# Kernel optimization log

Hardware: AMD Instinct MI355X
Metric: run time of the kernel (lower is better)

The kernel has to match this reference:

```python
import jax, jax.numpy as jnp
import numpy as np

N_X = 32640   # total xlmr subword tokens (64 seqs x 510 tokens)
N_S = 16320   # total stanza word tokens (2 subwords per word)
E = 65280     # dependency edges (bidirectional, avg degree ~4)
D = 768
GCN_DIM = 256
GCN_NUM = 2
POS_DIM = 4
N_UPOS = 17
N_LABEL = 5


def setup_inputs() -> dict:
    key = jax.random.key(0)
    ks = jax.random.split(key, 8)
    x = jax.random.normal(ks[0], (N_X, D), dtype=jnp.float32)
    # mapStanza2Xlmr as segment ids: xlmr token j belongs to stanza word j//2
    seg = jnp.arange(N_X, dtype=jnp.int32) // 2
    edge_index = jax.random.randint(ks[1], (2, E), 0, N_S, dtype=jnp.int32)
    upos_ids = jax.random.randint(ks[2], (N_S,), 0, N_UPOS, dtype=jnp.int32)
    Wc = jax.random.normal(ks[3], (D, GCN_DIM), dtype=jnp.float32) * 0.02
    bc = jnp.zeros((GCN_DIM,), dtype=jnp.float32)
    gcn_W = jax.random.normal(ks[4], (GCN_NUM, GCN_DIM, GCN_DIM), dtype=jnp.float32) * 0.05
    gcn_b = jnp.zeros((GCN_NUM, GCN_DIM), dtype=jnp.float32)
    upos_table = jax.random.normal(ks[5], (N_UPOS, POS_DIM), dtype=jnp.float32)
    Wcls = jax.random.normal(ks[6], (D + GCN_DIM + POS_DIM, N_LABEL), dtype=jnp.float32) * 0.02
    bcls = jnp.zeros((N_LABEL,), dtype=jnp.float32)
    return {"x": x, "seg": seg, "edge_index": edge_index, "upos_ids": upos_ids,
            "Wc": Wc, "bc": bc, "gcn_W": gcn_W, "gcn_b": gcn_b,
            "upos_table": upos_table, "Wcls": Wcls, "bcls": bcls}


def _gcn_conv(h, srcs, dsts, W, b, n):
    # PyG GCNConv: h' = D^-1/2 (A+I) D^-1/2 (h W) + b  (self loops already in srcs/dsts)
    h = h @ W
    deg = jax.ops.segment_sum(jnp.ones_like(dsts, h.dtype), dsts, num_segments=n)
    dinv = jax.lax.rsqrt(deg)  # deg >= 1 because of self loops
    coef = dinv[srcs] * dinv[dsts]
    out = jax.ops.segment_sum(h[srcs] * coef[:, None], dsts, num_segments=n)
    return out + b


def reference(x, seg, edge_index, upos_ids, Wc, bc, gcn_W, gcn_b, upos_table, Wcls, bcls):
    # mapStanza2Xlmr: mean-pool subword embeddings into stanza word embeddings
    cnt = jax.ops.segment_sum(jnp.ones((N_X,), x.dtype), seg, num_segments=N_S)
    stanza = jax.ops.segment_sum(x, seg, num_segments=N_S) / cnt[:, None]  # [N_S, D]
    # GCN over dependency edges (gcn_mode=0: biedges)
    h = stanza @ Wc + bc
    self_idx = jnp.arange(N_S, dtype=edge_index.dtype)
    srcs = jnp.concatenate([edge_index[0], self_idx])
    dsts = jnp.concatenate([edge_index[1], self_idx])
    for i in range(GCN_NUM):
        h = jax.nn.relu(_gcn_conv(h, srcs, dsts, gcn_W[i], gcn_b[i], N_S))
    # POS embedding + concat + relu
    pos = upos_table[upos_ids]                                  # [N_S, POS_DIM]
    info = jax.nn.relu(jnp.concatenate([h, pos], axis=1))       # [N_S, GCN_DIM+POS_DIM]
    # mapXlmr2Stanza: each subword gathers its (single) word's info
    append = info[seg]                                          # [N_X, GCN_DIM+POS_DIM]
    tok = jnp.concatenate([x, append], axis=1)                  # [N_X, 1028]
    logits = jax.nn.relu(tok) @ Wcls + bcls
    return jax.nn.log_softmax(logits, axis=1)
```

## Files before the change

### kernel.cpp

```cpp
#include <hip/hip_runtime.h>

#define NXT 32640
#define NS  16320
#define NE  65280
#define DD  768
#define GD  256
#define NLAB 5
#define CAP 32

typedef __attribute__((ext_vector_type(8))) short bf16x8;
typedef __attribute__((ext_vector_type(8))) unsigned short u16x8;
typedef __attribute__((ext_vector_type(4))) float f32x4;
typedef __attribute__((ext_vector_type(8))) float f32x8;

__device__ inline unsigned short f2b(float f) {
    unsigned int u = __float_as_uint(f);
    unsigned int r = (u + 0x7FFFu + ((u >> 16) & 1u)) >> 16;
    return (unsigned short)r;
}
__device__ inline float b2f(unsigned short h) {
    return __uint_as_float((unsigned int)h << 16);
}
__device__ inline int swz(int c) { return c ^ ((c >> 4) & 7); }

__device__ inline void tile_transpose(const float* __restrict__ src, unsigned short* __restrict__ dst,
                                      int K, int k0, int n0, int tid) {
    __shared__ unsigned short tl[64][65];
#pragma unroll
    for (int i = 0; i < 16; ++i) {
        int idx = tid + i * 256;
        int r = idx >> 6, c = idx & 63;
        tl[r][c] = f2b(src[(size_t)(k0 + r) * GD + n0 + c]);
    }
    __syncthreads();
#pragma unroll
    for (int i = 0; i < 16; ++i) {
        int idx = tid + i * 256;
        int rr = idx >> 6, cc = idx & 63;
        dst[(size_t)(n0 + rr) * K + k0 + cc] = tl[cc][rr];
    }
}

__global__ void k_setup(int* __restrict__ cnt,
                        const float* __restrict__ Wc, unsigned short* __restrict__ WcT,
                        const float* __restrict__ gcn_W, unsigned short* __restrict__ WT,
                        const float* __restrict__ Wcls, float* __restrict__ WclsT,
                        const float* __restrict__ upos_table, const float* __restrict__ bcls,
                        float* __restrict__ posLogit) {
    int b = blockIdx.x, t = threadIdx.x;
    if (b < 64) {
        int i = b * 256 + t;
        if (i < NS) cnt[i] = 0;
    } else if (b < 112) {
        int tile = b - 64;
        tile_transpose(Wc, WcT, DD, (tile >> 2) * 64, (tile & 3) * 64, t);
    } else if (b < 128) {
        int tile = b - 112;
        tile_transpose(gcn_W, WT, GD, (tile >> 2) * 64, (tile & 3) * 64, t);
    } else if (b < 144) {
        int tile = b - 128;
        tile_transpose(gcn_W + (size_t)GD * GD, WT + (size_t)GD * GD, GD,
                       (tile >> 2) * 64, (tile & 3) * 64, t);
    } else if (b < 159) {
        int idx = (b - 144) * 256 + t;
        if (idx < NLAB * DD) {
            int l = idx / DD, k = idx - l * DD;
            WclsT[idx] = Wcls[(size_t)k * NLAB + l];
        }
    } else {
        if (t < 17 * NLAB) {
            int u = t / NLAB, l = t - u * NLAB;
            float a = bcls[l];
#pragma unroll
            for (int p = 0; p < 4; ++p) {
                float pv = upos_table[u * 4 + p];
                pv = pv > 0.f ? pv : 0.f;
                a += pv * Wcls[(size_t)(DD + GD + p) * NLAB + l];
            }
            posLogit[t] = a;
        }
    }
}

__global__ __launch_bounds__(512, 2) void k_mega0(const float* __restrict__ x,
                                                  const unsigned short* __restrict__ WcT,
                                                  const float* __restrict__ WclsT,
                                                  const float* __restrict__ bc,
                                                  const int* __restrict__ ei,
                                                  int* __restrict__ cnt, int* __restrict__ csr_src,
                                                  unsigned short* __restrict__ h_bf,
                                                  float* __restrict__ partial) {
    __shared__ unsigned short lds[1536 * 8];
    const int tid = threadIdx.x;
    if (blockIdx.x >= 512) {
        int e = (blockIdx.x - 512) * 512 + tid;
        if (e < NE) {
            int dst = ei[NE + e];
            int slot = atomicAdd(&cnt[dst], 1);
            if (slot < CAP) csr_src[(size_t)dst * CAP + slot] = ei[e];
        }
        return;
    }
    const int xcd = blockIdx.x & 7, slot = blockIdx.x >> 3;
    const int bm64 = (slot >> 1) * 8 + xcd;
    const int bn   = slot & 1;
    if (bm64 >= 255) return;
    const int bm = bm64 * 64;

    const int lane = tid & 63;
    const int wv   = tid >> 6;
    const int wr   = wv & 3, wc = wv >> 2;

    const int kc = tid & 7, rl = (tid >> 3) & 15, g = tid >> 7;
    const int w_loc = g * 16 + rl;
    const float* xr0 = x + (size_t)(2 * (bm + w_loc)) * DD + kc * 8;
    const float* xr1 = xr0 + DD;
    const int aw_slot = swz((kc >> 2) * 256 + g * 64 + (kc & 3) * 16 + rl);
    const float* wcl = WclsT + kc * 8;

    const unsigned short* srcB[2];
#pragma unroll
    for (int q = 0; q < 2; ++q) {
        int s = q * 512 + tid;
        int gran = s >> 8, chunk = s & 255;
        int nh = gran >> 1, kh = gran & 1;
        int rg = chunk >> 6, kc2 = (chunk >> 4) & 3, rl2 = chunk & 15;
        srcB[q] = WcT + (size_t)(bn * 128 + nh * 64 + rg * 16 + rl2) * DD + kh * 32 + kc2 * 8;
    }

    const bf16x8* ldsv = (const bf16x8*)lds;
    f32x4 acc[4] = {};
    float lg0[NLAB] = {}, lg1[NLAB] = {};

    f32x8 va = *(const f32x8*)xr0;
    f32x8 vb = *(const f32x8*)xr1;

    for (int it = 0; it < 12; ++it) {
        const int k0 = it * 64;
#pragma unroll
        for (int q = 0; q < 2; ++q)
            __builtin_amdgcn_global_load_lds(srcB[q] + k0, lds + (size_t)(512 + q * 512 + tid) * 8, 16, 0, 0);
        u16x8 pool;
#pragma unroll
        for (int i = 0; i < 8; ++i) pool[i] = f2b((va[i] + vb[i]) * 0.5f);
        *(u16x8*)(lds + (size_t)aw_slot * 8) = pool;
        if (bn == 0) {
#pragma unroll
            for (int l = 0; l < NLAB; ++l) {
                f32x8 wv8 = *(const f32x8*)(wcl + (size_t)l * DD + k0);
#pragma unroll
                for (int i = 0; i < 8; ++i) {
                    float ra = va[i] > 0.f ? va[i] : 0.f;
                    float rb = vb[i] > 0.f ? vb[i] : 0.f;
                    lg0[l] += ra * wv8[i];
                    lg1[l] += rb * wv8[i];
                }
            }
        }
        f32x8 va_n = va, vb_n = vb;
        if (it < 11) {
            va_n = *(const f32x8*)(xr0 + k0 + 64);
            vb_n = *(const f32x8*)(xr1 + k0 + 64);
        }
        __syncthreads();
#pragma unroll
        for (int kh = 0; kh < 2; ++kh) {
            bf16x8 a = ldsv[swz(kh * 256 + wr * 64 + lane)];
#pragma unroll
            for (int n = 0; n < 4; ++n) {
                bf16x8 b = ldsv[512 + (wc * 2 + kh) * 256 + n * 64 + lane];
                acc[n] = __builtin_amdgcn_mfma_f32_16x16x32_bf16(a, b, acc[n], 0, 0, 0);
            }
        }
        __syncthreads();
        va = va_n; vb = vb_n;
    }

    const int rl2 = lane & 15, rq = lane >> 4;
    {
        int row0 = bm + wr * 16 + rq * 4;
#pragma unroll
        for (int n = 0; n < 4; ++n) {
            int col = bn * 128 + wc * 64 + n * 16 + rl2;
            float bv = bc[col];
#pragma unroll
            for (int r = 0; r < 4; ++r)
                h_bf[(size_t)(row0 + r) * GD + col] = f2b(acc[n][r] + bv);
        }
    }

    if (bn == 0) {
#pragma unroll
        for (int l = 0; l < NLAB; ++l) {
            lg0[l] += __shfl_xor(lg0[l], 1); lg0[l] += __shfl_xor(lg0[l], 2); lg0[l] += __shfl_xor(lg0[l], 4);
            lg1[l] += __shfl_xor(lg1[l], 1); lg1[l] += __shfl_xor(lg1[l], 2); lg1[l] += __shfl_xor(lg1[l], 4);
        }
        if (kc == 0) {
            int w = bm + w_loc;
            float* pp = partial + (size_t)w * 2 * NLAB;
#pragma unroll
            for (int l = 0; l < NLAB; ++l) { pp[l] = lg0[l]; pp[NLAB + l] = lg1[l]; }
        }
    }
}

__global__ __launch_bounds__(256) void k_gemm(const unsigned short* __restrict__ A,
                                              const unsigned short* __restrict__ BT,
                                              const float* __restrict__ bias,
                                              unsigned short* __restrict__ out,
                                              int K, int nbn) {
    __shared__ unsigned short lds[1536 * 8];
    const int tid  = threadIdx.x;
    const int lane = tid & 63;
    const int wv   = tid >> 6;
    const int wr   = wv >> 1, wc = wv & 1;
    const int bm   = (blockIdx.x / nbn) * 64;
    const int bn   = (blockIdx.x % nbn) * 128;

    const int g  = tid >> 6, w_ = tid & 63, kc = w_ >> 4, rl = w_ & 15;
    const unsigned short* srcA  = A  + (size_t)(bm + g * 16 + rl) * K + kc * 8;
    const unsigned short* srcB0 = BT + (size_t)(bn      + g * 16 + rl) * K + kc * 8;
    const unsigned short* srcB1 = BT + (size_t)(bn + 64 + g * 16 + rl) * K + kc * 8;

    unsigned short* dA0 = lds + (size_t)tid * 8;
    unsigned short* dA1 = dA0 + 256 * 8;
    unsigned short* dB  = lds + (size_t)(512 + tid) * 8;

    const bf16x8* fA = (const bf16x8*)lds + (wr * 2) * 64 + lane;
    const bf16x8* fB = (const bf16x8*)lds + 512 + wc * 256 + lane;

    f32x4 acc[2][4] = {};
    for (int k0 = 0; k0 < K; k0 += 64) {
        __builtin_amdgcn_global_load_lds(srcA  + k0,      dA0,            16, 0, 0);
        __builtin_amdgcn_global_load_lds(srcA  + k0 + 32, dA1,            16, 0, 0);
        __builtin_amdgcn_global_load_lds(srcB0 + k0,      dB,             16, 0, 0);
        __builtin_amdgcn_global_load_lds(srcB1 + k0,      dB + 256 * 8,   16, 0, 0);
        __builtin_amdgcn_global_load_lds(srcB0 + k0 + 32, dB + 512 * 8,   16, 0, 0);
        __builtin_amdgcn_global_load_lds(srcB1 + k0 + 32, dB + 768 * 8,   16, 0, 0);
        __syncthreads();
#pragma unroll
        for (int kh = 0; kh < 2; ++kh) {
            bf16x8 a0 = fA[kh * 256], a1 = fA[kh * 256 + 64];
            const bf16x8* fb = fB + kh * 512;
            bf16x8 b0 = fb[0], b1 = fb[64], b2 = fb[128], b3 = fb[192];
            acc[0][0] = __builtin_amdgcn_mfma_f32_16x16x32_bf16(a0, b0, acc[0][0], 0, 0, 0);
            acc[0][1] = __builtin_amdgcn_mfma_f32_16x16x32_bf16(a0, b1, acc[0][1], 0, 0, 0);
            acc[0][2] = __builtin_amdgcn_mfma_f32_16x16x32_bf16(a0, b2, acc[0][2], 0, 0, 0);
            acc[0][3] = __builtin_amdgcn_mfma_f32_16x16x32_bf16(a0, b3, acc[0][3], 0, 0, 0);
            acc[1][0] = __builtin_amdgcn_mfma_f32_16x16x32_bf16(a1, b0, acc[1][0], 0, 0, 0);
            acc[1][1] = __builtin_amdgcn_mfma_f32_16x16x32_bf16(a1, b1, acc[1][1], 0, 0, 0);
            acc[1][2] = __builtin_amdgcn_mfma_f32_16x16x32_bf16(a1, b2, acc[1][2], 0, 0, 0);
            acc[1][3] = __builtin_amdgcn_mfma_f32_16x16x32_bf16(a1, b3, acc[1][3], 0, 0, 0);
        }
        __syncthreads();
    }

    const int rl2 = lane & 15, rq = lane >> 4;
#pragma unroll
    for (int m = 0; m < 2; ++m) {
        int row0 = bm + wr * 32 + m * 16 + rq * 4;
#pragma unroll
        for (int n = 0; n < 4; ++n) {
            int col = bn + wc * 64 + n * 16 + rl2;
            float bv = bias ? bias[col] : 0.f;
#pragma unroll
            for (int r = 0; r < 4; ++r)
                out[(size_t)(row0 + r) * GD + col] = f2b(acc[m][n][r] + bv);
        }
    }
}

__global__ void k_gather(const int* __restrict__ cnt, const int* __restrict__ csr_src,
                         const unsigned short* __restrict__ hW,
                         const float* __restrict__ b, unsigned short* __restrict__ hout) {
    int w    = blockIdx.x * 4 + (threadIdx.x >> 6);
    int lane = threadIdx.x & 63;
    int c = cnt[w];
    float dw = rsqrtf((float)c + 1.0f);
    const int* sl = csr_src + (size_t)w * CAP;
    float ax = 0.f, ay = 0.f, az = 0.f, aw = 0.f;
    for (int j = 0; j < c; ++j) {
        int src = sl[j];
        float cf = rsqrtf((float)cnt[src] + 1.0f) * dw;
        ushort4 v = *(const ushort4*)&hW[(size_t)src * GD + lane * 4];
        ax += cf * b2f(v.x); ay += cf * b2f(v.y); az += cf * b2f(v.z); aw += cf * b2f(v.w);
    }
    ushort4 sv = *(const ushort4*)&hW[(size_t)w * GD + lane * 4];
    f32x4 bv = *(const f32x4*)&b[lane * 4];
    float c2 = dw * dw;
    float rx = ax + b2f(sv.x) * c2 + bv[0];
    float ry = ay + b2f(sv.y) * c2 + bv[1];
    float rz = az + b2f(sv.z) * c2 + bv[2];
    float rw = aw + b2f(sv.w) * c2 + bv[3];
    ushort4 o;
    o.x = f2b(rx > 0.f ? rx : 0.f);
    o.y = f2b(ry > 0.f ? ry : 0.f);
    o.z = f2b(rz > 0.f ? rz : 0.f);
    o.w = f2b(rw > 0.f ? rw : 0.f);
    *(ushort4*)&hout[(size_t)w * GD + lane * 4] = o;
}

__global__ void k_gather_final(const int* __restrict__ cnt, const int* __restrict__ csr_src,
                               const unsigned short* __restrict__ hW,
                               const float* __restrict__ b,
                               const float* __restrict__ partial,
                               const int* __restrict__ upos_ids,
                               const float* __restrict__ posLogit,
                               const float* __restrict__ Wcls,
                               float* __restrict__ out) {
    int w    = blockIdx.x * 4 + (threadIdx.x >> 6);
    int lane = threadIdx.x & 63;
    int c = cnt[w];
    float dw = rsqrtf((float)c + 1.0f);
    const int* sl = csr_src + (size_t)w * CAP;
    float ax = 0.f, ay = 0.f, az = 0.f, aw = 0.f;
    for (int j = 0; j < c; ++j) {
        int src = sl[j];
        float cf = rsqrtf((float)cnt[src] + 1.0f) * dw;
        ushort4 v = *(const ushort4*)&hW[(size_t)src * GD + lane * 4];
        ax += cf * b2f(v.x); ay += cf * b2f(v.y); az += cf * b2f(v.z); aw += cf * b2f(v.w);
    }
    ushort4 sv = *(const ushort4*)&hW[(size_t)w * GD + lane * 4];
    f32x4 bv = *(const f32x4*)&b[lane * 4];
    float c2 = dw * dw;
    float hv[4];
    hv[0] = ax + b2f(sv.x) * c2 + bv[0];
    hv[1] = ay + b2f(sv.y) * c2 + bv[1];
    hv[2] = az + b2f(sv.z) * c2 + bv[2];
    hv[3] = aw + b2f(sv.w) * c2 + bv[3];
    float acc[NLAB] = {};
#pragma unroll
    for (int i = 0; i < 4; ++i) {
        float v = hv[i] > 0.f ? hv[i] : 0.f;
        const float* wr = Wcls + (size_t)(DD + lane * 4 + i) * NLAB;
#pragma unroll
        for (int l = 0; l < NLAB; ++l) acc[l] += v * wr[l];
    }
#pragma unroll
    for (int off = 32; off > 0; off >>= 1)
#pragma unroll
        for (int l = 0; l < NLAB; ++l) acc[l] += __shfl_xor(acc[l], off);
    if (lane == 0) {
        const float* pl = posLogit + (size_t)upos_ids[w] * NLAB;
        const float* pp = partial + (size_t)w * 2 * NLAB;
#pragma unroll
        for (int t = 0; t < 2; ++t) {
            float lg[NLAB];
#pragma unroll
            for (int l = 0; l < NLAB; ++l) lg[l] = acc[l] + pp[t * NLAB + l] + pl[l];
            float m = lg[0];
#pragma unroll
            for (int l = 1; l < NLAB; ++l) m = fmaxf(m, lg[l]);
            float s = 0.f;
#pragma unroll
            for (int l = 0; l < NLAB; ++l) s += __expf(lg[l] - m);
            float lse = __logf(s) + m;
            float* op = out + (size_t)(2 * w + t) * NLAB;
#pragma unroll
            for (int l = 0; l < NLAB; ++l) op[l] = lg[l] - lse;
        }
    }
}

extern "C" void kernel_launch(void* const* d_in, const int* in_sizes, int n_in,
                              void* d_out, int out_size, void* d_ws, size_t ws_size,
                              hipStream_t stream) {
    const float* x          = (const float*)d_in[0];
    const int*   ei         = (const int*)d_in[2];
    const int*   upos_ids   = (const int*)d_in[3];
    const float* Wc         = (const float*)d_in[4];
    const float* bc         = (const float*)d_in[5];
    const float* gcn_W      = (const float*)d_in[6];
    const float* gcn_b      = (const float*)d_in[7];
    const float* upos_table = (const float*)d_in[8];
    const float* Wcls       = (const float*)d_in[9];
    const float* bcls       = (const float*)d_in[10];
    float* out = (float*)d_out;

    char* ws = (char*)d_ws;
    float* partial          = (float*)ws;            ws += (size_t)NXT * NLAB * 4;
    float* WclsT            = (float*)ws;            ws += (size_t)NLAB * DD * 4;
    float* posLogit         = (float*)ws;            ws += (size_t)17 * NLAB * 4;
    unsigned short* h_bf    = (unsigned short*)ws;   ws += (size_t)NS * GD * 2;
    unsigned short* hW_bf   = (unsigned short*)ws;   ws += (size_t)NS * GD * 2;
    unsigned short* WcT     = (unsigned short*)ws;   ws += (size_t)DD * GD * 2;
    unsigned short* WT      = (unsigned short*)ws;   ws += (size_t)2 * GD * GD * 2;
    int* cnt                = (int*)ws;              ws += (size_t)NS * 4;
    int* csr_src            = (int*)ws;              ws += (size_t)NS * CAP * 4;

    k_setup<<<160, 256, 0, stream>>>(cnt, Wc, WcT, gcn_W, WT, Wcls, WclsT,
                                     upos_table, bcls, posLogit);
    k_mega0<<<640, 512, 0, stream>>>(x, WcT, WclsT, bc, ei, cnt, csr_src, h_bf, partial);
    k_gemm<<<(NS / 64) * 2, 256, 0, stream>>>(h_bf, WT, nullptr, hW_bf, GD, 2);
    k_gather<<<NS / 4, 256, 0, stream>>>(cnt, csr_src, hW_bf, gcn_b, h_bf);
    k_gemm<<<(NS / 64) * 2, 256, 0, stream>>>(h_bf, WT + (size_t)GD * GD, nullptr, hW_bf, GD, 2);
    k_gather_final<<<NS / 4, 256, 0, stream>>>(cnt, csr_src, hW_bf, gcn_b + GD,
                                               partial, upos_ids, posLogit, Wcls, out);
}
```

Measured before the change: 111.5 us.

## Retile fused pool+GEMM kernel to 256-thread blocks with 64x64 tiles and K=32 steps

Restructures the first fused kernel from 512-thread blocks computing 64x128 output tiles over K=64 steps into 256-thread blocks computing 64x64 tiles over K=32 steps, with four column blocks per row tile. The block-to-XCD mapping changes so each XCD covers a contiguous range of row tiles, and the LDS swizzle is dropped. The aim is higher occupancy and better cache locality per XCD. The cost is twice as many loop iterations and barriers, and x rows are pooled and read by four blocks instead of two.

```diff
diff --git a/kernel.cpp b/kernel.cpp
--- a/kernel.cpp
+++ b/kernel.cpp
@@ -21,7 +21,6 @@
 __device__ inline float b2f(unsigned short h) {
     return __uint_as_float((unsigned int)h << 16);
 }
-__device__ inline int swz(int c) { return c ^ ((c >> 4) & 7); }
 
 __device__ inline void tile_transpose(const float* __restrict__ src, unsigned short* __restrict__ dst,
                                       int K, int k0, int n0, int tid) {
@@ -82,7 +81,7 @@
     }
 }
 
-__global__ __launch_bounds__(512, 2) void k_mega0(const float* __restrict__ x,
+__global__ __launch_bounds__(256, 4) void k_mega0(const float* __restrict__ x,
                                                   const unsigned short* __restrict__ WcT,
                                                   const float* __restrict__ WclsT,
                                                   const float* __restrict__ bc,
@@ -90,10 +89,10 @@
                                                   int* __restrict__ cnt, int* __restrict__ csr_src,
                                                   unsigned short* __restrict__ h_bf,
                                                   float* __restrict__ partial) {
-    __shared__ unsigned short lds[1536 * 8];
+    __shared__ unsigned short lds[512 * 8];
     const int tid = threadIdx.x;
-    if (blockIdx.x >= 512) {
-        int e = (blockIdx.x - 512) * 512 + tid;
+    if (blockIdx.x >= 1024) {
+        int e = (blockIdx.x - 1024) * 256 + tid;
         if (e < NE) {
             int dst = ei[NE + e];
             int slot = atomicAdd(&cnt[dst], 1);
@@ -101,32 +100,24 @@
         }
         return;
     }
-    const int xcd = blockIdx.x & 7, slot = blockIdx.x >> 3;
-    const int bm64 = (slot >> 1) * 8 + xcd;
-    const int bn   = slot & 1;
+    const int xcd = blockIdx.x & 7, seq = blockIdx.x >> 3;
+    const int bm64 = xcd * 32 + (seq >> 2);
+    const int bn   = seq & 3;
     if (bm64 >= 255) return;
     const int bm = bm64 * 64;
 
     const int lane = tid & 63;
     const int wv   = tid >> 6;
-    const int wr   = wv & 3, wc = wv >> 2;
-
-    const int kc = tid & 7, rl = (tid >> 3) & 15, g = tid >> 7;
+
+    const int kc = tid & 3, rl = (tid >> 2) & 15, g = tid >> 6;
     const int w_loc = g * 16 + rl;
     const float* xr0 = x + (size_t)(2 * (bm + w_loc)) * DD + kc * 8;
     const float* xr1 = xr0 + DD;
-    const int aw_slot = swz((kc >> 2) * 256 + g * 64 + (kc & 3) * 16 + rl);
+    const int aw_slot = g * 64 + kc * 16 + rl;
     const float* wcl = WclsT + kc * 8;
 
-    const unsigned short* srcB[2];
-#pragma unroll
-    for (int q = 0; q < 2; ++q) {
-        int s = q * 512 + tid;
-        int gran = s >> 8, chunk = s & 255;
-        int nh = gran >> 1, kh = gran & 1;
-        int rg = chunk >> 6, kc2 = (chunk >> 4) & 3, rl2 = chunk & 15;
-        srcB[q] = WcT + (size_t)(bn * 128 + nh * 64 + rg * 16 + rl2) * DD + kh * 32 + kc2 * 8;
-    }
+    const int bn_ = tid >> 6, c_ = tid & 63, kq = c_ >> 4, cl = c_ & 15;
+    const unsigned short* srcB = WcT + (size_t)(bn * 64 + bn_ * 16 + cl) * DD + kq * 8;
 
     const bf16x8* ldsv = (const bf16x8*)lds;
     f32x4 acc[4] = {};
@@ -135,11 +126,9 @@
     f32x8 va = *(const f32x8*)xr0;
     f32x8 vb = *(const f32x8*)xr1;
 
-    for (int it = 0; it < 12; ++it) {
-        const int k0 = it * 64;
-#pragma unroll
-        for (int q = 0; q < 2; ++q)
-            __builtin_amdgcn_global_load_lds(srcB[q] + k0, lds + (size_t)(512 + q * 512 + tid) * 8, 16, 0, 0);
+    for (int it = 0; it < 24; ++it) {
+        const int k0 = it * 32;
+        __builtin_amdgcn_global_load_lds(srcB + k0, lds + (size_t)(256 + tid) * 8, 16, 0, 0);
         u16x8 pool;
 #pragma unroll
         for (int i = 0; i < 8; ++i) pool[i] = f2b((va[i] + vb[i]) * 0.5f);
@@ -158,17 +147,16 @@
             }
         }
         f32x8 va_n = va, vb_n = vb;
-        if (it < 11) {
-            va_n = *(const f32x8*)(xr0 + k0 + 64);
-            vb_n = *(const f32x8*)(xr1 + k0 + 64);
+        if (it < 23) {
+            va_n = *(const f32x8*)(xr0 + k0 + 32);
+            vb_n = *(const f32x8*)(xr1 + k0 + 32);
         }
         __syncthreads();
-#pragma unroll
-        for (int kh = 0; kh < 2; ++kh) {
-            bf16x8 a = ldsv[swz(kh * 256 + wr * 64 + lane)];
+        {
+            bf16x8 a = ldsv[wv * 64 + lane];
 #pragma unroll
             for (int n = 0; n < 4; ++n) {
-                bf16x8 b = ldsv[512 + (wc * 2 + kh) * 256 + n * 64 + lane];
+                bf16x8 b = ldsv[256 + n * 64 + lane];
                 acc[n] = __builtin_amdgcn_mfma_f32_16x16x32_bf16(a, b, acc[n], 0, 0, 0);
             }
         }
@@ -178,10 +166,10 @@
 
     const int rl2 = lane & 15, rq = lane >> 4;
     {
-        int row0 = bm + wr * 16 + rq * 4;
+        int row0 = bm + wv * 16 + rq * 4;
 #pragma unroll
         for (int n = 0; n < 4; ++n) {
-            int col = bn * 128 + wc * 64 + n * 16 + rl2;
+            int col = bn * 64 + n * 16 + rl2;
             float bv = bc[col];
 #pragma unroll
             for (int r = 0; r < 4; ++r)
@@ -192,8 +180,8 @@
     if (bn == 0) {
 #pragma unroll
         for (int l = 0; l < NLAB; ++l) {
-            lg0[l] += __shfl_xor(lg0[l], 1); lg0[l] += __shfl_xor(lg0[l], 2); lg0[l] += __shfl_xor(lg0[l], 4);
-            lg1[l] += __shfl_xor(lg1[l], 1); lg1[l] += __shfl_xor(lg1[l], 2); lg1[l] += __shfl_xor(lg1[l], 4);
+            lg0[l] += __shfl_xor(lg0[l], 1); lg0[l] += __shfl_xor(lg0[l], 2);
+            lg1[l] += __shfl_xor(lg1[l], 1); lg1[l] += __shfl_xor(lg1[l], 2);
         }
         if (kc == 0) {
             int w = bm + w_loc;
@@ -390,7 +378,7 @@
 
     k_setup<<<160, 256, 0, stream>>>(cnt, Wc, WcT, gcn_W, WT, Wcls, WclsT,
                                      upos_table, bcls, posLogit);
-    k_mega0<<<640, 512, 0, stream>>>(x, WcT, WclsT, bc, ei, cnt, csr_src, h_bf, partial);
+    k_mega0<<<1279, 256, 0, stream>>>(x, WcT, WclsT, bc, ei, cnt, csr_src, h_bf, partial);
     k_gemm<<<(NS / 64) * 2, 256, 0, stream>>>(h_bf, WT, nullptr, hW_bf, GD, 2);
     k_gather<<<NS / 4, 256, 0, stream>>>(cnt, csr_src, hW_bf, gcn_b, h_bf);
     k_gemm<<<(NS / 64) * 2, 256, 0, stream>>>(h_bf, WT + (size_t)GD * GD, nullptr, hW_bf, GD, 2);
```

Result: slower. 131.6 us (+18.1%).
